# Optimization experiments

Hardware: AMD Instinct MI355X
Metric: run time of the kernel (lower is better)

Reference implementation:

```python
import jax, jax.numpy as jnp
import numpy as np

B, N, E, D, L, NC = 48, 96, 1024, 300, 4, 7
NEG = 1e30


def _gru(x, h, w_ih, w_hh, b_ih, b_hh):
    # torch.nn.GRUCell math; weights are (3D, D) in torch layout
    gi = x @ w_ih.T + b_ih
    gh = h @ w_hh.T + b_hh
    ir, iz, inn = jnp.split(gi, 3, axis=-1)
    hr, hz, hn = jnp.split(gh, 3, axis=-1)
    r = jax.nn.sigmoid(ir + hr)
    z = jax.nn.sigmoid(iz + hz)
    n = jnp.tanh(inn + r * hn)
    return (1.0 - z) * n + z * h


def _layer(Cin, Hin, adj, cwi, cwh, cbi, cbh, pwi, pwh, pbi, pbh, wq, wk, gb):
    b, n, d = Cin.shape
    zeros = jnp.zeros((b, d), Cin.dtype)
    c0 = _gru(Cin[:, 0], zeros, cwi, cwh, cbi, cbh)          # GRUCell with h=0
    p0 = _gru(zeros, Cin[:, 0], pwi, pwh, pbi, pbh)          # M=0 at step 0
    P0 = jnp.zeros_like(Cin).at[:, 0].set(p0)                # growing P kept as full buffer
    pos = jnp.arange(n)

    def step(P, i):
        q = Cin[:, i]                                        # (B, D)
        mask = adj[:, i] * (pos < i).astype(adj.dtype)       # only predecessors j < i
        # GatLinear: Linear(cat(Q,K)) == Q.wq + K.wk + b
        alpha = (q @ wq)[:, None] + P @ wk + gb              # (B, N)
        alpha = alpha - (1.0 - mask) * NEG                   # mask_logic
        w = jax.nn.softmax(alpha, axis=-1)
        M = jnp.einsum('bn,bnd->bd', w, P)
        c_i = _gru(q, M, cwi, cwh, cbi, cbh)
        p_i = _gru(M, Hin[:, i], pwi, pwh, pbi, pbh)
        P = jax.lax.dynamic_update_slice(P, p_i[:, None, :], (0, i, 0))
        return P, c_i

    P, Cs = jax.lax.scan(step, P0, jnp.arange(1, n))
    CL = jnp.concatenate([c0[:, None], jnp.moveaxis(Cs, 0, 1)], axis=1)  # (B, N, D)
    return CL, P


def reference(features, adj, s_mask, fc1_w, fc1_b,
              gc_wih, gc_whh, gc_bih, gc_bhh,
              gp_wih, gp_whh, gp_bih, gp_bhh,
              gat_wq, gat_wk, gat_b,
              mlp_w0, mlp_b0, mlp_w1, mlp_b1, mlp_w2, mlp_b2):
    # s_mask is unused when no_rel_attn=True (faithful to torch forward)
    H0 = jax.nn.relu(features @ fc1_w + fc1_b)
    H_list = [H0]
    C_list = [H0]
    for l in range(L):
        CL, P = _layer(C_list[l], H_list[l], adj,
                       gc_wih[l], gc_whh[l], gc_bih[l], gc_bhh[l],
                       gp_wih[l], gp_whh[l], gp_bih[l], gp_bhh[l],
                       gat_wq[l], gat_wk[l], gat_b[l])
        C_list.append(CL)
        H_list.append(CL)
        H_list.append(P)
    H_list.append(features)
    H = jnp.concatenate(H_list, axis=2)                      # (B, N, 9D + E)
    x = jax.nn.relu(H @ mlp_w0 + mlp_b0)
    x = jax.nn.relu(x @ mlp_w1 + mlp_b1)
    logits = x @ mlp_w2 + mlp_b2                             # (B, N, NC)
    return logits


def setup_inputs() -> dict:
    key = jax.random.key(0)
    ks = jax.random.split(key, 25)
    s = 0.02

    def p(k, shape):
        return jax.random.normal(k, shape, jnp.float32) * s

    features = jax.random.normal(ks[0], (B, N, E), jnp.float32)
    # DAG adjacency: random predecessors, strictly lower-triangular, previous
    # utterance always connected (guarantees a nonempty attention context)
    base = jax.random.bernoulli(ks[1], 0.5, (B, N, N)).astype(jnp.float32)
    tri = jnp.tril(jnp.ones((N, N), jnp.float32), -1)
    prev = jnp.eye(N, k=-1, dtype=jnp.float32)
    adj = jnp.maximum(base * tri, prev[None])
    s_mask = jax.random.randint(ks[2], (B, N, N), 0, 2, jnp.int32)
    in_dim = D * (2 * L + 1) + E
    return {
        'features': features, 'adj': adj, 's_mask': s_mask,
        'fc1_w': p(ks[3], (E, D)), 'fc1_b': p(ks[4], (D,)),
        'gc_wih': p(ks[5], (L, 3 * D, D)), 'gc_whh': p(ks[6], (L, 3 * D, D)),
        'gc_bih': p(ks[7], (L, 3 * D)), 'gc_bhh': p(ks[8], (L, 3 * D)),
        'gp_wih': p(ks[9], (L, 3 * D, D)), 'gp_whh': p(ks[10], (L, 3 * D, D)),
        'gp_bih': p(ks[11], (L, 3 * D)), 'gp_bhh': p(ks[12], (L, 3 * D)),
        'gat_wq': p(ks[13], (L, D)), 'gat_wk': p(ks[14], (L, D)), 'gat_b': p(ks[15], (L,)),
        'mlp_w0': p(ks[16], (in_dim, D)), 'mlp_b0': p(ks[17], (D,)),
        'mlp_w1': p(ks[18], (D, D)), 'mlp_b1': p(ks[19], (D,)),
        'mlp_w2': p(ks[20], (D, NC)), 'mlp_b2': p(ks[21], (NC,)),
    }
```

## Files before the change

### kernel.cpp

```cpp
#include <hip/hip_runtime.h>
#include <math.h>

#define BB 48
#define NN 96
#define EE 1024
#define DD 300
#define LL 4
#define G3 900
#define PP 150
#define PP2 152
#define NC4 38
#define HDIM 3724
#define ROWS (BB*NN)
#define NEGI -1.0e30f
#define KP300 304
#define GIC_TILES 540

#define NLDS 6
#define NPIN 14

typedef _Float16 half2_t __attribute__((ext_vector_type(2)));
typedef _Float16 h8 __attribute__((ext_vector_type(8)));
typedef float f4 __attribute__((ext_vector_type(4)));

__device__ __forceinline__ float sigm(float x){
    return __fdividef(1.0f, 1.0f + __expf(-x));
}
__device__ __forceinline__ float ftanh(float x){
    float e = __expf(2.0f*x);
    return 1.0f - __fdividef(2.0f, e + 1.0f);
}

__device__ __forceinline__ void dot4(const h8 wv, const h8 mc,
                                     float& a0, float& a1, float& a2, float& a3)
{
    half2_t w0,w1,w2,w3,m0,m1,m2,m3;
    w0.x=wv[0]; w0.y=wv[1]; m0.x=mc[0]; m0.y=mc[1];
    w1.x=wv[2]; w1.y=wv[3]; m1.x=mc[2]; m1.y=mc[3];
    w2.x=wv[4]; w2.y=wv[5]; m2.x=mc[4]; m2.y=mc[5];
    w3.x=wv[6]; w3.y=wv[7]; m3.x=mc[6]; m3.y=mc[7];
    a0 = __builtin_amdgcn_fdot2(w0, m0, a0, false);
    a1 = __builtin_amdgcn_fdot2(w1, m1, a1, false);
    a2 = __builtin_amdgcn_fdot2(w2, m2, a2, false);
    a3 = __builtin_amdgcn_fdot2(w3, m3, a3, false);
}

__global__ __launch_bounds__(256) void pack_w_q(const float* __restrict__ src_all,
                                                h8* __restrict__ dst)
{
    int l = blockIdx.y;
    int idx = blockIdx.x*256 + threadIdx.x;
    if (idx >= NC4*G3) return;
    int c = idx / G3, gate = idx % G3;
    const float* src = src_all + (size_t)l*G3*DD + (size_t)gate*DD;
    h8 v;
    #pragma unroll
    for (int j=0;j<8;j++){
        int d = 8*c + j;
        v[j] = (d<DD) ? (_Float16)src[d] : (_Float16)0.f;
    }
    dst[(size_t)l*NC4*G3 + idx] = v;
}

__global__ __launch_bounds__(256) void conv_gru_w(const float* __restrict__ gp_whh,
                                                  const float* __restrict__ gc_wih,
                                                  const float* __restrict__ gc_whh,
                                                  _Float16* __restrict__ outp)
{
    int z = blockIdx.y; int l = z/3, wsel = z%3;
    const float* src = (wsel==0?gp_whh:wsel==1?gc_wih:gc_whh) + (size_t)l*G3*DD;
    _Float16* dst = outp + (size_t)z*G3*KP300;
    int idx = blockIdx.x*256 + threadIdx.x;
    if (idx >= G3*KP300) return;
    int n = idx/KP300, k = idx%KP300;
    dst[idx] = (k<DD) ? (_Float16)src[(size_t)n*DD+k] : (_Float16)0.f;
}

__global__ __launch_bounds__(256) void convT(const float* __restrict__ src,
                                             _Float16* __restrict__ dst,
                                             int K, int N, int Kpad)
{
    int idx = blockIdx.x*256 + threadIdx.x;
    if (idx >= N*Kpad) return;
    int n = idx/Kpad, k = idx%Kpad;
    dst[idx] = (k<K) ? (_Float16)src[(size_t)k*N + n] : (_Float16)0.f;
}

__device__ __forceinline__ void gemm_tile(
    int m0, int n0, int tid,
    const float* __restrict__ A, int lda,
    const _Float16* __restrict__ B, int Kpad,
    const float* __restrict__ bias,
    float* __restrict__ C, int ldc,
    int N, int K, int relu,
    _Float16 (*As)[40], _Float16 (*Bs)[40])
{
    int w = tid>>6, lane = tid&63;
    int wy = w>>1, wx = w&1;
    int lm = lane&15, q = lane>>4;

    f4 acc[4][2];
    #pragma unroll
    for (int a=0;a<4;a++)
        #pragma unroll
        for (int b=0;b<2;b++)
            #pragma unroll
            for (int r=0;r<4;r++) acc[a][b][r]=0.f;

    int am = tid>>1, akg = (tid&1)*16;
    int bn = tid>>2, bkg = (tid&3)*8;
    const float* arow = A + (size_t)(m0+am)*lda;

    for (int k0=0; k0<K; k0+=32){
        {
            __align__(16) _Float16 av[16];
            #pragma unroll
            for (int u=0;u<16;u+=4){
                int k = k0 + akg + u;
                float x0,x1,x2,x3;
                if (k+4 <= K){
                    float4 v = *(const float4*)(arow + k);
                    x0=v.x;x1=v.y;x2=v.z;x3=v.w;
                } else {
                    x0 = (k  <K)? arow[k  ]:0.f;
                    x1 = (k+1<K)? arow[k+1]:0.f;
                    x2 = (k+2<K)? arow[k+2]:0.f;
                    x3 = (k+3<K)? arow[k+3]:0.f;
                }
                av[u]=(_Float16)x0; av[u+1]=(_Float16)x1;
                av[u+2]=(_Float16)x2; av[u+3]=(_Float16)x3;
            }
            *(h8*)&As[am][akg]   = *(h8*)&av[0];
            *(h8*)&As[am][akg+8] = *(h8*)&av[8];
        }
        {
            int gk = k0 + bkg;
            h8 bv;
            #pragma unroll
            for (int j=0;j<8;j++) bv[j]=(_Float16)0.f;
            if (n0+bn < N && gk < Kpad)
                bv = *(const h8*)(B + (size_t)(n0+bn)*Kpad + gk);
            *(h8*)&Bs[bn][bkg] = bv;
        }
        __syncthreads();
        h8 af[4], bf[2];
        #pragma unroll
        for (int mb=0; mb<4; mb++) af[mb] = *(h8*)&As[wy*64+mb*16+lm][q*8];
        #pragma unroll
        for (int nb=0; nb<2; nb++) bf[nb] = *(h8*)&Bs[wx*32+nb*16+lm][q*8];
        #pragma unroll
        for (int mb=0; mb<4; mb++)
            #pragma unroll
            for (int nb=0; nb<2; nb++)
                acc[mb][nb] = __builtin_amdgcn_mfma_f32_16x16x32_f16(af[mb], bf[nb], acc[mb][nb], 0,0,0);
        __syncthreads();
    }
    #pragma unroll
    for (int mb=0; mb<4; mb++){
        int r0 = m0 + wy*64 + mb*16 + q*4;
        #pragma unroll
        for (int nb=0; nb<2; nb++){
            int c = n0 + wx*32 + nb*16 + lm;
            if (c < N){
                float bb = bias[c];
                #pragma unroll
                for (int reg=0; reg<4; reg++){
                    float v = acc[mb][nb][reg] + bb;
                    if (relu) v = fmaxf(v, 0.f);
                    C[(size_t)(r0+reg)*ldc + c] = v;
                }
            }
        }
    }
}

__global__ __launch_bounds__(256) void gemm_mfma(
    const float* __restrict__ A, int lda,
    const _Float16* __restrict__ B, int Kpad,
    const float* __restrict__ bias,
    float* __restrict__ C, int ldc,
    int N, int K, int relu)
{
    __shared__ _Float16 As[128][40];
    __shared__ _Float16 Bs[64][40];
    gemm_tile(blockIdx.y*128, blockIdx.x*64, threadIdx.x,
              A, lda, B, Kpad, bias, C, ldc, N, K, relu, As, Bs);
}

__global__ void featcopy(const float* __restrict__ f, float* __restrict__ H)
{
    size_t row = blockIdx.x;
    int t = threadIdx.x;
    float4 v = *(const float4*)(f + row*EE + t*4);
    *(float4*)(H + row*HDIM + 2700 + t*4) = v;
}

__global__ void __launch_bounds__(1024)
__attribute__((amdgpu_waves_per_eu(4,4)))
scan_kernel(
    float* __restrict__ Hbuf,
    const float* __restrict__ GHp,
    const h8* __restrict__ pwiQ,
    const h8* __restrict__ pwhQ,
    const float* __restrict__ pbi,
    const float* __restrict__ pbh,
    const float* __restrict__ wk,
    const float* __restrict__ wq,
    const float* __restrict__ gat_b, int lidx,
    const float* __restrict__ adj,
    float* __restrict__ Mbuf,
    int ccol, int hcol, int pcol,
    const _Float16* __restrict__ cwiF,
    const float* __restrict__ cbi,
    float* __restrict__ GIc)
{
    __shared__ __align__(16) char pool[160576];
    (void)wq; (void)gat_b; (void)lidx;

    if (blockIdx.x >= BB){
        if (threadIdx.x < 256){
            _Float16 (*As)[40] = (_Float16 (*)[40])pool;
            _Float16 (*Bs)[40] = (_Float16 (*)[40])(pool + 128*40*2);
            int bid = blockIdx.x - BB;
            int n0 = (bid % 15)*64, m0 = (bid / 15)*128;
            gemm_tile(m0, n0, threadIdx.x, Hbuf + ccol, HDIM, cwiF, KP300,
                      cbi, GIc, G3, G3, DD, 0, As, Bs);
        }
        return;
    }

    int b = blockIdx.x;
    int t = threadIdx.x;

    half2_t (*P_h2)[PP]   = (half2_t (*)[PP])(pool);
    h8*      Wlds         = (h8*)(pool + 57600);
    float*   g_s          = (float*)(pool + 144000);
    float  (*Mpart)[DD]   = (float (*)[DD])(pool + 147600);
    float*   ghp_s        = (float*)(pool + 152400);
    float*   hv_s         = (float*)(pool + 156000);
    half2_t* M_h2         = (half2_t*)(pool + 157200);
    float*   pk_s         = (float*)(pool + 157840);
    float*   pksum        = (float*)(pool + 158224);
    float2*  cpair        = (float2*)(pool + 158256);
    int*     ncnt_s       = (int*)(pool + 159024);
    unsigned (*adjb)[4]   = (unsigned (*)[4])(pool + 159040);

    size_t rowbase = (size_t)b*NN;

    float pbi_r = (t < G3) ? pbi[t] : 0.f;
    float2 wk_r = make_float2(0.f,0.f);
    if (t < PP) wk_r = *(const float2*)&wk[2*t];

    h8 wp0,wp1,wp2,wp3,wp4,wp5,wp6,wp7,wp8,wp9,wp10,wp11,wp12,wp13;
    if (t < G3){
        const h8* W = pwiQ + t;
        wp0 = W[(size_t)6*G3];   wp1 = W[(size_t)7*G3];   wp2 = W[(size_t)8*G3];
        wp3 = W[(size_t)9*G3];   wp4 = W[(size_t)10*G3];  wp5 = W[(size_t)11*G3];
        wp6 = W[(size_t)12*G3];  wp7 = W[(size_t)13*G3];  wp8 = W[(size_t)14*G3];
        wp9 = W[(size_t)15*G3];  wp10 = W[(size_t)16*G3]; wp11 = W[(size_t)17*G3];
        wp12 = W[(size_t)18*G3]; wp13 = W[(size_t)19*G3];
        asm volatile("" : "+v"(wp0),"+v"(wp1),"+v"(wp2),"+v"(wp3),
                          "+v"(wp4),"+v"(wp5),"+v"(wp6));
        asm volatile("" : "+v"(wp7),"+v"(wp8),"+v"(wp9),"+v"(wp10),
                          "+v"(wp11),"+v"(wp12),"+v"(wp13));
    }

    for (int idx=t; idx<NLDS*G3; idx+=1024)
        Wlds[idx] = pwiQ[idx];
    if (t < NN*3){
        int r = t/3, w = t%3;
        const float* arow = adj + (rowbase + r)*NN + w*32;
        unsigned m = 0;
        for (int c=0;c<32;c++) if (arow[c] != 0.f) m |= (1u<<c);
        adjb[r][w] = m;
    }
    if (t < PP){
        float2 c2 = *(const float2*)&Hbuf[rowbase*HDIM + ccol + 2*t];
        Mpart[0][2*t] = c2.x; Mpart[0][2*t+1] = c2.y;
        half2_t mh; mh.x = (_Float16)c2.x; mh.y = (_Float16)c2.y;
        M_h2[t] = mh;
    } else if (t < PP2){
        half2_t z; z.x=(_Float16)0.f; z.y=(_Float16)0.f;
        M_h2[t] = z;
    }
    __syncthreads();
    if (t < G3){
        const h8* W2 = pwhQ + t;
        float a0=0.f, a1=0.f, a2=0.f, a3=0.f;
        #pragma unroll 4
        for (int c=0;c<NC4;c++){
            h8 wv = W2[(size_t)c*G3];
            h8 mc = *(h8*)&M_h2[4*c];
            dot4(wv, mc, a0,a1,a2,a3);
        }
        g_s[t] = pbh[t] + (a0+a2) + (a1+a3);
    }
    __syncthreads();
    if (t < 192){
        float pw = 0.f;
        if (t < PP){
            int d0 = 2*t, d1 = 2*t+1;
            float r0  = sigm(pbi[d0]      + g_s[d0]);
            float z0  = sigm(pbi[DD+d0]   + g_s[DD+d0]);
            float n0  = ftanh(pbi[2*DD+d0] + r0*g_s[2*DD+d0]);
            float p0  = (1.f-z0)*n0 + z0*Mpart[0][d0];
            float r1  = sigm(pbi[d1]      + g_s[d1]);
            float z1  = sigm(pbi[DD+d1]   + g_s[DD+d1]);
            float n1  = ftanh(pbi[2*DD+d1] + r1*g_s[2*DD+d1]);
            float p1  = (1.f-z1)*n1 + z1*Mpart[0][d1];
            *(float2*)&Hbuf[rowbase*HDIM + pcol + d0] = make_float2(p0,p1);
            half2_t ph; ph.x = (_Float16)p0; ph.y = (_Float16)p1;
            P_h2[0][t] = ph;
            pw = p0*wk_r.x + p1*wk_r.y;
            *(float2*)&Mbuf[rowbase*DD + d0] = make_float2(0.f,0.f);
        }
        #pragma unroll
        for (int o=32;o>0;o>>=1) pw += __shfl_xor(pw,o);
        if ((t&63)==0) pksum[t>>6] = pw;
    }
    __syncthreads();

    float m_run = NEGI;

    for (int i=1;i<NN;i++){
        size_t row = rowbase + i;
        if (t < 64){
            float s_last = pksum[0]+pksum[1]+pksum[2];
            if (t==0) pk_s[i-1] = s_last;
            m_run = fmaxf(m_run, s_last);
            bool act0 = false, act1 = false;
            float a0 = NEGI, a1 = NEGI;
            if (t < i && ((adjb[i][t>>5]>>(t&31))&1u)){
                act0 = true;
                a0 = (t==i-1)? s_last : pk_s[t];
            }
            int j1 = 64+t;
            if (t < 32 && j1 < i && ((adjb[i][2]>>t)&1u)){
                act1 = true;
                a1 = (j1==i-1)? s_last : pk_s[j1];
            }
            float e0 = act0 ? __expf(a0 - m_run) : 0.f;
            float e1 = act1 ? __expf(a1 - m_run) : 0.f;
            float ss = e0+e1;
            #pragma unroll
            for (int o=32;o>0;o>>=1) ss += __shfl_xor(ss,o);
            float inv = __fdividef(1.f, ss);
            unsigned long long mask0 = __ballot(act0);
            unsigned long long mask1 = __ballot(act1);
            unsigned long long lt = (1ull<<t)-1ull;
            int base = __popcll(mask0);
            if (act0){
                int pos0 = __popcll(mask0 & lt);
                cpair[pos0] = make_float2(__int_as_float(t), e0*inv);
            }
            if (act1){
                int pos1 = base + __popcll(mask1 & lt);
                cpair[pos1] = make_float2(__int_as_float(j1), e1*inv);
            }
            if (t==0) ncnt_s[0] = base + __popcll(mask1);
        }
        __syncthreads();
        if (t < 600){
            int nact = ncnt_s[0];
            int g = t/150, dp = t%150;
            int cnt = (nact+3)>>2;
            int j0 = g*cnt; int jend = j0+cnt; if (jend > nact) jend = nact;
            float m0=0.f, m1=0.f;
            #pragma unroll 4
            for (int jj=j0;jj<jend;jj++){
                float2 pr = cpair[jj];
                int j = __float_as_int(pr.x);
                half2_t pv = P_h2[j][dp];
                m0 += pr.y*(float)pv.x;
                m1 += pr.y*(float)pv.y;
            }
            *(float2*)&Mpart[g][2*dp] = make_float2(m0,m1);
        }
        __syncthreads();
        if (t < PP){
            float m0 = Mpart[0][2*t]+Mpart[1][2*t]+Mpart[2][2*t]+Mpart[3][2*t];
            float m1 = Mpart[0][2*t+1]+Mpart[1][2*t+1]+Mpart[2][2*t+1]+Mpart[3][2*t+1];
            half2_t mh; mh.x = (_Float16)m0; mh.y = (_Float16)m1;
            M_h2[t] = mh;
            *(float2*)&Mbuf[row*DD + 2*t] = make_float2(m0,m1);
        }
        __syncthreads();
        if (t < G3){
            const h8* W = pwiQ + t;
            const h8* Mc = (const h8*)M_h2;
            float a0=0.f, a1=0.f, a2=0.f, a3=0.f;
            dot4(Wlds[t],        Mc[0], a0,a1,a2,a3);
            dot4(Wlds[G3+t],     Mc[1], a0,a1,a2,a3);
            dot4(Wlds[2*G3+t],   Mc[2], a0,a1,a2,a3);
            dot4(Wlds[3*G3+t],   Mc[3], a0,a1,a2,a3);
            dot4(Wlds[4*G3+t],   Mc[4], a0,a1,a2,a3);
            dot4(Wlds[5*G3+t],   Mc[5], a0,a1,a2,a3);
            dot4(wp0,  Mc[6],  a0,a1,a2,a3);
            dot4(wp1,  Mc[7],  a0,a1,a2,a3);
            dot4(wp2,  Mc[8],  a0,a1,a2,a3);
            dot4(wp3,  Mc[9],  a0,a1,a2,a3);
            dot4(wp4,  Mc[10], a0,a1,a2,a3);
            dot4(wp5,  Mc[11], a0,a1,a2,a3);
            dot4(wp6,  Mc[12], a0,a1,a2,a3);
            dot4(wp7,  Mc[13], a0,a1,a2,a3);
            dot4(wp8,  Mc[14], a0,a1,a2,a3);
            dot4(wp9,  Mc[15], a0,a1,a2,a3);
            dot4(wp10, Mc[16], a0,a1,a2,a3);
            dot4(wp11, Mc[17], a0,a1,a2,a3);
            dot4(wp12, Mc[18], a0,a1,a2,a3);
            dot4(wp13, Mc[19], a0,a1,a2,a3);
            #pragma unroll 6
            for (int c=NLDS+NPIN;c<NC4;c++){
                h8 wv = W[(size_t)c*G3];
                dot4(wv, Mc[c], a0,a1,a2,a3);
            }
            g_s[t] = pbi_r + (a0+a2) + (a1+a3);
        } else if (t >= 960){
            int k = t - 960;
            #pragma unroll
            for (int it2=0; it2<5; it2++){
                int idx = k + it2*64;
                if (idx < 225)
                    *(float4*)&ghp_s[idx*4] = *(const float4*)&GHp[row*G3 + idx*4];
                else if (idx < 300){
                    int h = idx-225;
                    *(float4*)&hv_s[h*4] = *(const float4*)&Hbuf[row*HDIM + hcol + h*4];
                }
            }
        }
        __syncthreads();
        if (t < 192){
            float pw = 0.f;
            if (t < PP){
                int d0 = 2*t, d1 = 2*t+1;
                float2 hv = *(const float2*)&hv_s[d0];
                float r0  = sigm(g_s[d0]      + ghp_s[d0]);
                float z0  = sigm(g_s[DD+d0]   + ghp_s[DD+d0]);
                float n0  = ftanh(g_s[2*DD+d0] + r0*ghp_s[2*DD+d0]);
                float p0  = (1.f-z0)*n0 + z0*hv.x;
                float r1  = sigm(g_s[d1]      + ghp_s[d1]);
                float z1  = sigm(g_s[DD+d1]   + ghp_s[DD+d1]);
                float n1  = ftanh(g_s[2*DD+d1] + r1*ghp_s[2*DD+d1]);
                float p1  = (1.f-z1)*n1 + z1*hv.y;
                *(float2*)&Hbuf[row*HDIM + pcol + d0] = make_float2(p0,p1);
                half2_t ph; ph.x = (_Float16)p0; ph.y = (_Float16)p1;
                P_h2[i][t] = ph;
                pw = p0*wk_r.x + p1*wk_r.y;
            }
            #pragma unroll
            for (int o=32;o>0;o>>=1) pw += __shfl_xor(pw,o);
            if ((t&63)==0) pksum[t>>6] = pw;
        }
        __syncthreads();
    }
}

__global__ __launch_bounds__(320) void combine_c(
    const float* __restrict__ GIc, const float* __restrict__ GHc,
    const float* __restrict__ Mbuf, float* __restrict__ Hbuf, int clcol)
{
    size_t row = blockIdx.x;
    int d = threadIdx.x;
    if (d < DD){
        float ir = GIc[row*G3+d], iz = GIc[row*G3+DD+d], inn = GIc[row*G3+2*DD+d];
        float hr = GHc[row*G3+d], hz = GHc[row*G3+DD+d], hn  = GHc[row*G3+2*DD+d];
        float r  = sigm(ir+hr);
        float z  = sigm(iz+hz);
        float nn = ftanh(inn + r*hn);
        float h  = Mbuf[row*DD+d];
        Hbuf[row*HDIM + clcol + d] = (1.f-z)*nn + z*h;
    }
}

__global__ __launch_bounds__(64) void logits_kernel(
    const float* __restrict__ x2, const float* __restrict__ w2,
    const float* __restrict__ b2, float* __restrict__ out)
{
    size_t row = blockIdx.x;
    int lane = threadIdx.x;
    float acc[7]={0,0,0,0,0,0,0};
    for (int d=lane; d<DD; d+=64){
        float x = x2[row*DD+d];
        #pragma unroll
        for (int c=0;c<7;c++) acc[c] += x*w2[d*7+c];
    }
    #pragma unroll
    for (int c=0;c<7;c++){
        float s = acc[c];
        #pragma unroll
        for (int o=32;o>0;o>>=1) s += __shfl_down(s,o);
        if (lane==0) out[row*7+c] = s + b2[c];
    }
}

extern "C" void kernel_launch(void* const* d_in, const int* in_sizes, int n_in,
                              void* d_out, int out_size, void* d_ws, size_t ws_size,
                              hipStream_t stream)
{
    const float* features = (const float*)d_in[0];
    const float* adj      = (const float*)d_in[1];
    const float* fc1_w    = (const float*)d_in[3];
    const float* fc1_b    = (const float*)d_in[4];
    const float* gc_wih   = (const float*)d_in[5];
    const float* gc_whh   = (const float*)d_in[6];
    const float* gc_bih   = (const float*)d_in[7];
    const float* gc_bhh   = (const float*)d_in[8];
    const float* gp_wih   = (const float*)d_in[9];
    const float* gp_whh   = (const float*)d_in[10];
    const float* gp_bih   = (const float*)d_in[11];
    const float* gp_bhh   = (const float*)d_in[12];
    const float* gat_wq   = (const float*)d_in[13];
    const float* gat_wk   = (const float*)d_in[14];
    const float* gat_b    = (const float*)d_in[15];
    const float* mlp_w0   = (const float*)d_in[16];
    const float* mlp_b0   = (const float*)d_in[17];
    const float* mlp_w1   = (const float*)d_in[18];
    const float* mlp_b1   = (const float*)d_in[19];
    const float* mlp_w2   = (const float*)d_in[20];
    const float* mlp_b2   = (const float*)d_in[21];
    float* out = (float*)d_out;

    float* ws = (float*)d_ws;
    size_t off = 0;
    float* Hbuf = ws + off; off += (size_t)ROWS*HDIM;
    float* bufA = ws + off; off += (size_t)ROWS*G3;
    float* bufB = ws + off; off += (size_t)ROWS*G3;
    float* bufC = ws + off; off += (size_t)ROWS*G3;
    float* Mbuf = ws + off; off += (size_t)ROWS*DD;
    h8* pwiQ = (h8*)(ws + off); off += (size_t)LL*NC4*G3*4;
    h8* pwhQ = (h8*)(ws + off); off += (size_t)LL*NC4*G3*4;
    _Float16* gruF = (_Float16*)(ws + off); off += (size_t)12*G3*KP300/2;
    _Float16* fc1F = (_Float16*)(ws + off); off += (size_t)DD*EE/2;
    _Float16* mlp0F= (_Float16*)(ws + off); off += (size_t)DD*3728/2;
    _Float16* mlp1F= (_Float16*)(ws + off); off += (size_t)DD*KP300/2;
    (void)ws_size; (void)in_sizes; (void)n_in; (void)out_size;

    {
        pack_w_q<<<dim3((NC4*G3+255)/256, LL), 256, 0, stream>>>(gp_wih, pwiQ);
        pack_w_q<<<dim3((NC4*G3+255)/256, LL), 256, 0, stream>>>(gp_whh, pwhQ);
        conv_gru_w<<<dim3((G3*KP300+255)/256, 12), 256, 0, stream>>>(gp_whh, gc_wih, gc_whh, gruF);
        convT<<<(DD*EE+255)/256, 256, 0, stream>>>(fc1_w, fc1F, EE, DD, EE);
        convT<<<(DD*3728+255)/256, 256, 0, stream>>>(mlp_w0, mlp0F, HDIM, DD, 3728);
        convT<<<(DD*KP300+255)/256, 256, 0, stream>>>(mlp_w1, mlp1F, DD, DD, KP300);
    }
    gemm_mfma<<<dim3(5,36),256,0,stream>>>(features, EE, fc1F, EE, fc1_b,
                                           Hbuf, HDIM, DD, EE, 1);
    featcopy<<<ROWS,256,0,stream>>>(features, Hbuf);

    for (int l=0;l<LL;l++){
        int ccol  = (l==0)? 0 : 300 + (l-1)*600;
        int hcol  = l*300;
        int pcol  = 600 + l*600;
        int clcol = 300 + l*600;
        const h8* pwiQl = pwiQ + (size_t)l*NC4*G3;
        const h8* pwhQl = pwhQ + (size_t)l*NC4*G3;
        const _Float16* pwhF = gruF + (size_t)(l*3+0)*G3*KP300;
        const _Float16* cwiF = gruF + (size_t)(l*3+1)*G3*KP300;
        const _Float16* cwhF = gruF + (size_t)(l*3+2)*G3*KP300;

        gemm_mfma<<<dim3(15,36),256,0,stream>>>(Hbuf+hcol, HDIM, pwhF, KP300,
                                                gp_bhh + l*G3, bufA, G3, G3, DD, 0);
        scan_kernel<<<BB+GIC_TILES,1024,0,stream>>>(Hbuf, bufA, pwiQl, pwhQl,
                                          gp_bih + l*G3, gp_bhh + l*G3,
                                          gat_wk + l*DD, gat_wq + l*DD, gat_b, l,
                                          adj, Mbuf, ccol, hcol, pcol,
                                          cwiF, gc_bih + l*G3, bufB);
        gemm_mfma<<<dim3(15,36),256,0,stream>>>(Mbuf, DD, cwhF, KP300,
                                                gc_bhh + l*G3, bufC, G3, G3, DD, 0);
        combine_c<<<ROWS,320,0,stream>>>(bufB, bufC, Mbuf, Hbuf, clcol);
    }

    gemm_mfma<<<dim3(5,36),256,0,stream>>>(Hbuf, HDIM, mlp0F, 3728, mlp_b0,
                                           bufB, DD, DD, HDIM, 1);
    gemm_mfma<<<dim3(5,36),256,0,stream>>>(bufB, DD, mlp1F, KP300, mlp_b1,
                                           bufC, DD, DD, DD, 1);
    logits_kernel<<<ROWS,64,0,stream>>>(bufC, mlp_w2, mlp_b2, out);
}
```

Baseline: 2.815 ms.

## Halve scan block to 512 threads with two GRU rows per thread

The scan kernel now runs with 512 threads per block instead of 1024. Each of the first 450 threads computes two of the 900 GRU gate outputs, and each keeps 22 rather than 14 weight chunks pinned in registers, so fewer weight reads go to global memory on every step. The attention-weighted sum is split three ways instead of four, and the GHp/Hin prefetch moves into the same phase as that sum. The cost is higher register pressure at two waves per EU and fewer threads to hide latency; the gemm_tile side-blocks still use only 256 threads.

```diff
diff --git a/kernel.cpp b/kernel.cpp
--- a/kernel.cpp
+++ b/kernel.cpp
@@ -17,7 +17,7 @@
 #define GIC_TILES 540
 
 #define NLDS 6
-#define NPIN 14
+#define NPIN 22
 
 typedef _Float16 half2_t __attribute__((ext_vector_type(2)));
 typedef _Float16 h8 __attribute__((ext_vector_type(8)));
@@ -195,8 +195,8 @@
     *(float4*)(H + row*HDIM + 2700 + t*4) = v;
 }
 
-__global__ void __launch_bounds__(1024)
-__attribute__((amdgpu_waves_per_eu(4,4)))
+__global__ void __launch_bounds__(512)
+__attribute__((amdgpu_waves_per_eu(2,2)))
 scan_kernel(
     float* __restrict__ Hbuf,
     const float* __restrict__ GHp,
@@ -214,7 +214,7 @@
     const float* __restrict__ cbi,
     float* __restrict__ GIc)
 {
-    __shared__ __align__(16) char pool[160576];
+    __shared__ __align__(16) char pool[159424];
     (void)wq; (void)gat_b; (void)lidx;
 
     if (blockIdx.x >= BB){
@@ -236,36 +236,66 @@
     h8*      Wlds         = (h8*)(pool + 57600);
     float*   g_s          = (float*)(pool + 144000);
     float  (*Mpart)[DD]   = (float (*)[DD])(pool + 147600);
-    float*   ghp_s        = (float*)(pool + 152400);
-    float*   hv_s         = (float*)(pool + 156000);
-    half2_t* M_h2         = (half2_t*)(pool + 157200);
-    float*   pk_s         = (float*)(pool + 157840);
-    float*   pksum        = (float*)(pool + 158224);
-    float2*  cpair        = (float2*)(pool + 158256);
-    int*     ncnt_s       = (int*)(pool + 159024);
-    unsigned (*adjb)[4]   = (unsigned (*)[4])(pool + 159040);
+    float*   ghp_s        = (float*)(pool + 151200);
+    float*   hv_s         = (float*)(pool + 154800);
+    half2_t* M_h2         = (half2_t*)(pool + 156000);
+    float*   pk_s         = (float*)(pool + 156640);
+    float*   pksum        = (float*)(pool + 157024);
+    float2*  cpair        = (float2*)(pool + 157056);
+    int*     ncnt_s       = (int*)(pool + 157824);
+    unsigned (*adjb)[4]   = (unsigned (*)[4])(pool + 157840);
 
     size_t rowbase = (size_t)b*NN;
 
-    float pbi_r = (t < G3) ? pbi[t] : 0.f;
+    float pbi_r0 = 0.f, pbi_r1 = 0.f;
+    if (t < 450){ pbi_r0 = pbi[t]; pbi_r1 = pbi[t+450]; }
     float2 wk_r = make_float2(0.f,0.f);
     if (t < PP) wk_r = *(const float2*)&wk[2*t];
 
-    h8 wp0,wp1,wp2,wp3,wp4,wp5,wp6,wp7,wp8,wp9,wp10,wp11,wp12,wp13;
-    if (t < G3){
-        const h8* W = pwiQ + t;
-        wp0 = W[(size_t)6*G3];   wp1 = W[(size_t)7*G3];   wp2 = W[(size_t)8*G3];
-        wp3 = W[(size_t)9*G3];   wp4 = W[(size_t)10*G3];  wp5 = W[(size_t)11*G3];
-        wp6 = W[(size_t)12*G3];  wp7 = W[(size_t)13*G3];  wp8 = W[(size_t)14*G3];
-        wp9 = W[(size_t)15*G3];  wp10 = W[(size_t)16*G3]; wp11 = W[(size_t)17*G3];
-        wp12 = W[(size_t)18*G3]; wp13 = W[(size_t)19*G3];
-        asm volatile("" : "+v"(wp0),"+v"(wp1),"+v"(wp2),"+v"(wp3),
-                          "+v"(wp4),"+v"(wp5),"+v"(wp6));
-        asm volatile("" : "+v"(wp7),"+v"(wp8),"+v"(wp9),"+v"(wp10),
-                          "+v"(wp11),"+v"(wp12),"+v"(wp13));
-    }
-
-    for (int idx=t; idx<NLDS*G3; idx+=1024)
+    h8 wa0,wa1,wa2,wa3,wa4,wa5,wa6,wa7,wa8,wa9,wa10,
+       wa11,wa12,wa13,wa14,wa15,wa16,wa17,wa18,wa19,wa20,wa21;
+    h8 wb0,wb1,wb2,wb3,wb4,wb5,wb6,wb7,wb8,wb9,wb10,
+       wb11,wb12,wb13,wb14,wb15,wb16,wb17,wb18,wb19,wb20,wb21;
+    if (t < 450){
+        const h8* W0 = pwiQ + t;
+        const h8* W1 = pwiQ + t + 450;
+        wa0 = W0[(size_t)6*G3];   wb0 = W1[(size_t)6*G3];
+        wa1 = W0[(size_t)7*G3];   wb1 = W1[(size_t)7*G3];
+        wa2 = W0[(size_t)8*G3];   wb2 = W1[(size_t)8*G3];
+        wa3 = W0[(size_t)9*G3];   wb3 = W1[(size_t)9*G3];
+        wa4 = W0[(size_t)10*G3];  wb4 = W1[(size_t)10*G3];
+        wa5 = W0[(size_t)11*G3];  wb5 = W1[(size_t)11*G3];
+        wa6 = W0[(size_t)12*G3];  wb6 = W1[(size_t)12*G3];
+        wa7 = W0[(size_t)13*G3];  wb7 = W1[(size_t)13*G3];
+        wa8 = W0[(size_t)14*G3];  wb8 = W1[(size_t)14*G3];
+        wa9 = W0[(size_t)15*G3];  wb9 = W1[(size_t)15*G3];
+        wa10 = W0[(size_t)16*G3]; wb10 = W1[(size_t)16*G3];
+        wa11 = W0[(size_t)17*G3]; wb11 = W1[(size_t)17*G3];
+        wa12 = W0[(size_t)18*G3]; wb12 = W1[(size_t)18*G3];
+        wa13 = W0[(size_t)19*G3]; wb13 = W1[(size_t)19*G3];
+        wa14 = W0[(size_t)20*G3]; wb14 = W1[(size_t)20*G3];
+        wa15 = W0[(size_t)21*G3]; wb15 = W1[(size_t)21*G3];
+        wa16 = W0[(size_t)22*G3]; wb16 = W1[(size_t)22*G3];
+        wa17 = W0[(size_t)23*G3]; wb17 = W1[(size_t)23*G3];
+        wa18 = W0[(size_t)24*G3]; wb18 = W1[(size_t)24*G3];
+        wa19 = W0[(size_t)25*G3]; wb19 = W1[(size_t)25*G3];
+        wa20 = W0[(size_t)26*G3]; wb20 = W1[(size_t)26*G3];
+        wa21 = W0[(size_t)27*G3]; wb21 = W1[(size_t)27*G3];
+        asm volatile("" : "+v"(wa0),"+v"(wa1),"+v"(wa2),"+v"(wa3),
+                          "+v"(wa4),"+v"(wa5),"+v"(wa6),"+v"(wa7));
+        asm volatile("" : "+v"(wa8),"+v"(wa9),"+v"(wa10),"+v"(wa11),
+                          "+v"(wa12),"+v"(wa13),"+v"(wa14),"+v"(wa15));
+        asm volatile("" : "+v"(wa16),"+v"(wa17),"+v"(wa18),"+v"(wa19),
+                          "+v"(wa20),"+v"(wa21));
+        asm volatile("" : "+v"(wb0),"+v"(wb1),"+v"(wb2),"+v"(wb3),
+                          "+v"(wb4),"+v"(wb5),"+v"(wb6),"+v"(wb7));
+        asm volatile("" : "+v"(wb8),"+v"(wb9),"+v"(wb10),"+v"(wb11),
+                          "+v"(wb12),"+v"(wb13),"+v"(wb14),"+v"(wb15));
+        asm volatile("" : "+v"(wb16),"+v"(wb17),"+v"(wb18),"+v"(wb19),
+                          "+v"(wb20),"+v"(wb21));
+    }
+
+    for (int idx=t; idx<NLDS*G3; idx+=512)
         Wlds[idx] = pwiQ[idx];
     if (t < NN*3){
         int r = t/3, w = t%3;
@@ -284,16 +314,20 @@
         M_h2[t] = z;
     }
     __syncthreads();
-    if (t < G3){
-        const h8* W2 = pwhQ + t;
-        float a0=0.f, a1=0.f, a2=0.f, a3=0.f;
-        #pragma unroll 4
+    if (t < 450){
+        const h8* W2a = pwhQ + t;
+        const h8* W2b = pwhQ + t + 450;
+        const h8* Mc = (const h8*)M_h2;
+        float a0=0.f,a1=0.f,a2=0.f,a3=0.f;
+        float c0=0.f,c1=0.f,c2=0.f,c3=0.f;
+        #pragma unroll 2
         for (int c=0;c<NC4;c++){
-            h8 wv = W2[(size_t)c*G3];
-            h8 mc = *(h8*)&M_h2[4*c];
-            dot4(wv, mc, a0,a1,a2,a3);
-        }
-        g_s[t] = pbh[t] + (a0+a2) + (a1+a3);
+            h8 mc = Mc[c];
+            dot4(W2a[(size_t)c*G3], mc, a0,a1,a2,a3);
+            dot4(W2b[(size_t)c*G3], mc, c0,c1,c2,c3);
+        }
+        g_s[t]     = pbh[t]     + (a0+a2) + (a1+a3);
+        g_s[t+450] = pbh[t+450] + (c0+c2) + (c1+c3);
     }
     __syncthreads();
     if (t < 192){
@@ -360,10 +394,10 @@
             if (t==0) ncnt_s[0] = base + __popcll(mask1);
         }
         __syncthreads();
-        if (t < 600){
+        if (t < 450){
             int nact = ncnt_s[0];
             int g = t/150, dp = t%150;
-            int cnt = (nact+3)>>2;
+            int cnt = (nact+2)/3;
             int j0 = g*cnt; int jend = j0+cnt; if (jend > nact) jend = nact;
             float m0=0.f, m1=0.f;
             #pragma unroll 4
@@ -375,51 +409,11 @@
                 m1 += pr.y*(float)pv.y;
             }
             *(float2*)&Mpart[g][2*dp] = make_float2(m0,m1);
-        }
-        __syncthreads();
-        if (t < PP){
-            float m0 = Mpart[0][2*t]+Mpart[1][2*t]+Mpart[2][2*t]+Mpart[3][2*t];
-            float m1 = Mpart[0][2*t+1]+Mpart[1][2*t+1]+Mpart[2][2*t+1]+Mpart[3][2*t+1];
-            half2_t mh; mh.x = (_Float16)m0; mh.y = (_Float16)m1;
-            M_h2[t] = mh;
-            *(float2*)&Mbuf[row*DD + 2*t] = make_float2(m0,m1);
-        }
-        __syncthreads();
-        if (t < G3){
-            const h8* W = pwiQ + t;
-            const h8* Mc = (const h8*)M_h2;
-            float a0=0.f, a1=0.f, a2=0.f, a3=0.f;
-            dot4(Wlds[t],        Mc[0], a0,a1,a2,a3);
-            dot4(Wlds[G3+t],     Mc[1], a0,a1,a2,a3);
-            dot4(Wlds[2*G3+t],   Mc[2], a0,a1,a2,a3);
-            dot4(Wlds[3*G3+t],   Mc[3], a0,a1,a2,a3);
-            dot4(Wlds[4*G3+t],   Mc[4], a0,a1,a2,a3);
-            dot4(Wlds[5*G3+t],   Mc[5], a0,a1,a2,a3);
-            dot4(wp0,  Mc[6],  a0,a1,a2,a3);
-            dot4(wp1,  Mc[7],  a0,a1,a2,a3);
-            dot4(wp2,  Mc[8],  a0,a1,a2,a3);
-            dot4(wp3,  Mc[9],  a0,a1,a2,a3);
-            dot4(wp4,  Mc[10], a0,a1,a2,a3);
-            dot4(wp5,  Mc[11], a0,a1,a2,a3);
-            dot4(wp6,  Mc[12], a0,a1,a2,a3);
-            dot4(wp7,  Mc[13], a0,a1,a2,a3);
-            dot4(wp8,  Mc[14], a0,a1,a2,a3);
-            dot4(wp9,  Mc[15], a0,a1,a2,a3);
-            dot4(wp10, Mc[16], a0,a1,a2,a3);
-            dot4(wp11, Mc[17], a0,a1,a2,a3);
-            dot4(wp12, Mc[18], a0,a1,a2,a3);
-            dot4(wp13, Mc[19], a0,a1,a2,a3);
-            #pragma unroll 6
-            for (int c=NLDS+NPIN;c<NC4;c++){
-                h8 wv = W[(size_t)c*G3];
-                dot4(wv, Mc[c], a0,a1,a2,a3);
-            }
-            g_s[t] = pbi_r + (a0+a2) + (a1+a3);
-        } else if (t >= 960){
-            int k = t - 960;
+        } else {
+            int k = t-450;
             #pragma unroll
             for (int it2=0; it2<5; it2++){
-                int idx = k + it2*64;
+                int idx = k + it2*62;
                 if (idx < 225)
                     *(float4*)&ghp_s[idx*4] = *(const float4*)&GHp[row*G3 + idx*4];
                 else if (idx < 300){
@@ -427,6 +421,66 @@
                     *(float4*)&hv_s[h*4] = *(const float4*)&Hbuf[row*HDIM + hcol + h*4];
                 }
             }
+        }
+        __syncthreads();
+        if (t < PP){
+            float m0 = Mpart[0][2*t]+Mpart[1][2*t]+Mpart[2][2*t];
+            float m1 = Mpart[0][2*t+1]+Mpart[1][2*t+1]+Mpart[2][2*t+1];
+            half2_t mh; mh.x = (_Float16)m0; mh.y = (_Float16)m1;
+            M_h2[t] = mh;
+            *(float2*)&Mbuf[row*DD + 2*t] = make_float2(m0,m1);
+        }
+        __syncthreads();
+        if (t < 450){
+            const h8* W0 = pwiQ + t;
+            const h8* W1 = pwiQ + t + 450;
+            const h8* Mc = (const h8*)M_h2;
+            float a0=0.f,a1=0.f,a2=0.f,a3=0.f;
+            float c0=0.f,c1=0.f,c2=0.f,c3=0.f;
+            dot4(Wlds[t],            Mc[0], a0,a1,a2,a3);
+            dot4(Wlds[t+450],        Mc[0], c0,c1,c2,c3);
+            dot4(Wlds[G3+t],         Mc[1], a0,a1,a2,a3);
+            dot4(Wlds[G3+t+450],     Mc[1], c0,c1,c2,c3);
+            dot4(Wlds[2*G3+t],       Mc[2], a0,a1,a2,a3);
+            dot4(Wlds[2*G3+t+450],   Mc[2], c0,c1,c2,c3);
+            dot4(Wlds[3*G3+t],       Mc[3], a0,a1,a2,a3);
+            dot4(Wlds[3*G3+t+450],   Mc[3], c0,c1,c2,c3);
+            dot4(Wlds[4*G3+t],       Mc[4], a0,a1,a2,a3);
+            dot4(Wlds[4*G3+t+450],   Mc[4], c0,c1,c2,c3);
+            dot4(Wlds[5*G3+t],       Mc[5], a0,a1,a2,a3);
+            dot4(Wlds[5*G3+t+450],   Mc[5], c0,c1,c2,c3);
+            dot4(wa0,  Mc[6],  a0,a1,a2,a3);  dot4(wb0,  Mc[6],  c0,c1,c2,c3);
+            dot4(wa1,  Mc[7],  a0,a1,a2,a3);  dot4(wb1,  Mc[7],  c0,c1,c2,c3);
+            dot4(wa2,  Mc[8],  a0,a1,a2,a3);  dot4(wb2,  Mc[8],  c0,c1,c2,c3);
+            dot4(wa3,  Mc[9],  a0,a1,a2,a3);  dot4(wb3,  Mc[9],  c0,c1,c2,c3);
+            dot4(wa4,  Mc[10], a0,a1,a2,a3);  dot4(wb4,  Mc[10], c0,c1,c2,c3);
+            dot4(wa5,  Mc[11], a0,a1,a2,a3);  dot4(wb5,  Mc[11], c0,c1,c2,c3);
+            dot4(wa6,  Mc[12], a0,a1,a2,a3);  dot4(wb6,  Mc[12], c0,c1,c2,c3);
+            dot4(wa7,  Mc[13], a0,a1,a2,a3);  dot4(wb7,  Mc[13], c0,c1,c2,c3);
+            dot4(wa8,  Mc[14], a0,a1,a2,a3);  dot4(wb8,  Mc[14], c0,c1,c2,c3);
+            dot4(wa9,  Mc[15], a0,a1,a2,a3);  dot4(wb9,  Mc[15], c0,c1,c2,c3);
+            dot4(wa10, Mc[16], a0,a1,a2,a3);  dot4(wb10, Mc[16], c0,c1,c2,c3);
+            dot4(wa11, Mc[17], a0,a1,a2,a3);  dot4(wb11, Mc[17], c0,c1,c2,c3);
+            dot4(wa12, Mc[18], a0,a1,a2,a3);  dot4(wb12, Mc[18], c0,c1,c2,c3);
+            dot4(wa13, Mc[19], a0,a1,a2,a3);  dot4(wb13, Mc[19], c0,c1,c2,c3);
+            dot4(wa14, Mc[20], a0,a1,a2,a3);  dot4(wb14, Mc[20], c0,c1,c2,c3);
+            dot4(wa15, Mc[21], a0,a1,a2,a3);  dot4(wb15, Mc[21], c0,c1,c2,c3);
+            dot4(wa16, Mc[22], a0,a1,a2,a3);  dot4(wb16, Mc[22], c0,c1,c2,c3);
+            dot4(wa17, Mc[23], a0,a1,a2,a3);  dot4(wb17, Mc[23], c0,c1,c2,c3);
+            dot4(wa18, Mc[24], a0,a1,a2,a3);  dot4(wb18, Mc[24], c0,c1,c2,c3);
+            dot4(wa19, Mc[25], a0,a1,a2,a3);  dot4(wb19, Mc[25], c0,c1,c2,c3);
+            dot4(wa20, Mc[26], a0,a1,a2,a3);  dot4(wb20, Mc[26], c0,c1,c2,c3);
+            dot4(wa21, Mc[27], a0,a1,a2,a3);  dot4(wb21, Mc[27], c0,c1,c2,c3);
+            #pragma unroll 5
+            for (int c=NLDS+NPIN;c<NC4;c++){
+                h8 wv  = W0[(size_t)c*G3];
+                h8 wv2 = W1[(size_t)c*G3];
+                h8 mc  = Mc[c];
+                dot4(wv,  mc, a0,a1,a2,a3);
+                dot4(wv2, mc, c0,c1,c2,c3);
+            }
+            g_s[t]     = pbi_r0 + (a0+a2) + (a1+a3);
+            g_s[t+450] = pbi_r1 + (c0+c2) + (c1+c3);
         }
         __syncthreads();
         if (t < 192){
@@ -560,7 +614,7 @@
 
         gemm_mfma<<<dim3(15,36),256,0,stream>>>(Hbuf+hcol, HDIM, pwhF, KP300,
                                                 gp_bhh + l*G3, bufA, G3, G3, DD, 0);
-        scan_kernel<<<BB+GIC_TILES,1024,0,stream>>>(Hbuf, bufA, pwiQl, pwhQl,
+        scan_kernel<<<BB+GIC_TILES,512,0,stream>>>(Hbuf, bufA, pwiQl, pwhQl,
                                           gp_bih + l*G3, gp_bhh + l*G3,
                                           gat_wk + l*DD, gat_wq + l*DD, gat_b, l,
                                           adj, Mbuf, ccol, hcol, pcol,
```

After: 3.223 ms. +14.5%, slower.
